# Kernel optimization log

Measured on AMD Instinct MI355X. Metric: run time of the kernel, lower is better.

Reference implementation:

```python
import jax, jax.numpy as jnp
import numpy as np

B, N, E = 8, 10000, 160000
F_IN, HID, EMB = 5, 128, 256
A_LAST, S_STEP = 10, 1


def _gcn_layer(x, src, dst, W, b, num_nodes):
    # PyG GCNConv: h = x @ W^T, add self-loops, symmetric norm, scatter-add, + bias
    h = x @ W.T
    loops = jnp.arange(num_nodes, dtype=src.dtype)
    src2 = jnp.concatenate([src, loops])
    dst2 = jnp.concatenate([dst, loops])
    deg = jax.ops.segment_sum(jnp.ones_like(dst2, dtype=h.dtype), dst2, num_segments=num_nodes)
    dinv = jnp.where(deg > 0, jax.lax.rsqrt(deg), 0.0)
    norm = dinv[src2] * dinv[dst2]                     # [E+N]
    msgs = h[src2] * norm[:, None]                     # gather + scale
    out = jax.ops.segment_sum(msgs, dst2, num_segments=num_nodes)
    return out + b


def setup_inputs() -> dict:
    key = jax.random.key(0)
    ks = jax.random.split(key, 14)
    graph_x = jax.random.normal(ks[0], (B, N, F_IN), dtype=jnp.float32)
    graph_edges = jax.random.randint(ks[1], (B, 2, E), 0, N, dtype=jnp.int64)
    position_seq = jax.random.randint(ks[2], (B,), 0, N, dtype=jnp.int64)
    available_moves = jax.random.randint(ks[3], (B, 4), 0, N, dtype=jnp.int64)
    actions = jax.random.normal(ks[4], (B, A_LAST), dtype=jnp.float32)
    steps = jax.random.normal(ks[5], (B, S_STEP), dtype=jnp.float32)

    def glorot(k, shape):
        fan_in = shape[-1]
        return jax.random.normal(k, shape, dtype=jnp.float32) / jnp.sqrt(jnp.float32(fan_in))

    proj_in = HID * 5 + A_LAST + S_STEP
    params = {
        'W1': glorot(ks[6], (HID, F_IN)), 'b1': jnp.zeros((HID,), jnp.float32),
        'W2': glorot(ks[7], (HID, HID)), 'b2': jnp.zeros((HID,), jnp.float32),
        'Wp1': glorot(ks[8], (EMB, proj_in)), 'bp1': jnp.zeros((EMB,), jnp.float32),
        'Wp2': glorot(ks[9], (EMB, EMB)), 'bp2': jnp.zeros((EMB,), jnp.float32),
    }
    return dict(graph_x=graph_x, graph_edges=graph_edges, position_seq=position_seq,
                available_moves=available_moves, actions=actions, steps=steps, **params)


def reference(graph_x, graph_edges, position_seq, available_moves, actions, steps,
              W1, b1, W2, b2, Wp1, bp1, Wp2, bp2):
    b, n, f = graph_x.shape
    num_nodes = b * n
    x = graph_x.reshape(num_nodes, f)
    addition = (jnp.arange(b, dtype=graph_edges.dtype) * n)
    ei = graph_edges + addition[:, None, None]          # [B,2,E]
    ei = jnp.swapaxes(ei, 0, 1).reshape(2, -1)          # [2, B*E]
    src, dst = ei[0], ei[1]
    position = position_seq + addition
    all_positions = jnp.concatenate(
        [available_moves + addition[:, None], position[:, None]], axis=1)  # [B,5]

    x = jax.nn.relu(_gcn_layer(x, src, dst, W1, b1, num_nodes))
    x = jax.nn.relu(_gcn_layer(x, src, dst, W2, b2, num_nodes))

    current_x = x[all_positions].reshape(b, -1)          # [B, 5*HID]
    current_x = jnp.concatenate([current_x, actions, steps], axis=-1)
    h = jax.nn.relu(current_x @ Wp1.T + bp1)
    return h @ Wp2.T + bp2
```

## Files before the change

kernel.cpp:

```cpp
#include <hip/hip_runtime.h>

#define NB 8
#define NN 10000
#define NE 160000
#define NNODES (NB*NN)
#define NEDGE (NB*NE)
#define FIN 5
#define HID 128
#define EMB 256
#define ALAST 10
#define PROJ_IN (HID*5 + ALAST + 1)
#define NPOS 40
#define E0CAP 256
#define TCAP (NPOS + NPOS*E0CAP)
#define E1C 128
#define NBLK ((NNODES+255)/256)

#define C_NT 0
#define C_E0(t) (8 + (t)*16)

__global__ void k_clear(int* __restrict__ markT, int* __restrict__ degCnt,
                        int* __restrict__ cnts, int* __restrict__ e1cnt) {
    int i = blockIdx.x*256 + threadIdx.x;
    if (i < NNODES) { markT[i] = -1; degCnt[i] = 0; }
    if (i < 1024) cnts[i] = 0;
    for (int j = i; j < TCAP*4; j += NNODES) e1cnt[j] = 0;
}

__global__ void k_mark(const int* __restrict__ avail, const int* __restrict__ pos,
                       int* __restrict__ markT, int* __restrict__ Tnodes,
                       int* __restrict__ cnts,
                       int* __restrict__ pos2t0, int* __restrict__ posNode) {
    int p = threadIdx.x;
    int n = 0;
    if (p < NPOS) {
        int b = p / 5, pi = p - b*5;
        int node = (pi < 4) ? avail[b*4 + pi] : pos[b];
        n = node + b*NN;
    }
    int firstIdx = p;
    for (int q = 0; q < NPOS; ++q) {
        int nq = __shfl(n, q, 64);
        if (p < NPOS && q < p && nq == n && firstIdx == p) firstIdx = q;
    }
    bool isFirst = (p < NPOS) && (firstIdx == p);
    unsigned long long bal = __ballot(isFirst);
    if (p < NPOS) {
        int slot = __popcll(bal & ((1ull << firstIdx) - 1ull));
        if (isFirst) {
            markT[n] = slot; Tnodes[slot] = n;
        }
        pos2t0[p] = slot; posNode[p] = n;
    }
    if (p == 0) cnts[C_NT] = __popcll(bal);
}

__global__ __launch_bounds__(256) void k_pass1(const int* __restrict__ edges,
        const int* __restrict__ markT, int* __restrict__ cnts,
        int* __restrict__ e0) {
    int idx = blockIdx.x*256 + threadIdx.x;
    int g = idx / (NE/4), w4 = idx - g*(NE/4);
    const int* base = edges + (size_t)g*2*NE;
    int4 d4 = ((const int4*)(base + NE))[w4];
    int gofs = g*NN;
    int dd[4] = {d4.x, d4.y, d4.z, d4.w};
    #pragma unroll
    for (int c = 0; c < 4; ++c) {
        int t0 = markT[gofs + dd[c]];
        if (t0 >= 0) {
            int s = base[4*w4 + c] + gofs;
            int k = atomicAdd(&cnts[C_E0(t0)], 1);
            if (k < E0CAP) e0[t0*E0CAP + k] = s;
        }
    }
}

__global__ __launch_bounds__(256) void k_dedup(const int* __restrict__ e0,
                        int* __restrict__ cnts, int* __restrict__ markT,
                        int* __restrict__ Tnodes) {
    __shared__ int lc, base;
    int t0 = blockIdx.x;
    if (threadIdx.x == 0) lc = 0;
    __syncthreads();
    int m = cnts[C_E0(t0)]; if (m > E0CAP) m = E0CAP;
    int s = -1, myIdx = -1;
    if ((int)threadIdx.x < m) {
        s = e0[t0*E0CAP + threadIdx.x];
        if (atomicCAS(&markT[s], -1, -2) == -1)
            myIdx = atomicAdd(&lc, 1);
    }
    __syncthreads();
    if (threadIdx.x == 0 && lc > 0) base = atomicAdd(&cnts[C_NT], lc);
    __syncthreads();
    if (myIdx >= 0) {
        int slot = base + myIdx;
        Tnodes[slot] = s;
        markT[s] = slot;
    }
}

__global__ __launch_bounds__(256) void k_pass2(const int* __restrict__ edges,
        int* __restrict__ markT, int* __restrict__ e1cnt, int* __restrict__ e1,
        int* __restrict__ degCnt) {
    int idx = blockIdx.x*256 + threadIdx.x;
    int g = idx / (NE/4), w4 = idx - g*(NE/4);
    const int* base = edges + (size_t)g*2*NE;
    int4 d4 = ((const int4*)(base + NE))[w4];
    int gofs = g*NN;
    int dd[4] = {d4.x, d4.y, d4.z, d4.w};
    #pragma unroll
    for (int c = 0; c < 4; ++c) {
        int d = gofs + dd[c];
        int ts = markT[d];
        if (ts >= 0) {
            int s = base[4*w4 + c] + gofs;
            int k = atomicAdd(&e1cnt[ts*4], 1);
            if (k < E1C) e1[(size_t)ts*E1C + k] = s;
            atomicAdd(&degCnt[d], 1);
            if (markT[s] == -1) markT[s] = -3;
        }
    }
}

__global__ __launch_bounds__(256) void k_pass3(const int* __restrict__ edges,
        const int* __restrict__ markT, int* __restrict__ degCnt) {
    int idx = blockIdx.x*256 + threadIdx.x;
    int g = idx / (NE/4), w4 = idx - g*(NE/4);
    int4 d4 = ((const int4*)(edges + (size_t)g*2*NE + NE))[w4];
    int gofs = g*NN;
    int dd[4] = {d4.x, d4.y, d4.z, d4.w};
    #pragma unroll
    for (int c = 0; c < 4; ++c) {
        int n = gofs + dd[c];
        if (markT[n] == -3) atomicAdd(&degCnt[n], 1);
    }
}

__global__ __launch_bounds__(256) void k_aggT(
        const int* __restrict__ e1cnt, const int* __restrict__ e1,
        const int* __restrict__ degCnt, const int* __restrict__ cnts,
        const float* __restrict__ xg, float* __restrict__ axT) {
    int slot = blockIdx.x*4 + (threadIdx.x >> 6);
    int lane = threadIdx.x & 63;
    int ntv = cnts[C_NT]; if (ntv > TCAP) ntv = TCAP;
    if (slot >= ntv) return;
    int m = e1cnt[slot*4]; if (m > E1C) m = E1C;
    float acc[FIN] = {0.f, 0.f, 0.f, 0.f, 0.f};
    for (int j = lane; j < m; j += 64) {
        int s = e1[(size_t)slot*E1C + j];
        float dv = rsqrtf(1.0f + (float)degCnt[s]);
        const float* xr = xg + (size_t)s*FIN;
        #pragma unroll
        for (int f = 0; f < FIN; ++f) acc[f] += xr[f]*dv;
    }
    #pragma unroll
    for (int f = 0; f < FIN; ++f) {
        #pragma unroll
        for (int d = 32; d; d >>= 1) acc[f] += __shfl_down(acc[f], d, 64);
    }
    if (lane == 0) {
        #pragma unroll
        for (int f = 0; f < FIN; ++f) axT[(size_t)slot*FIN + f] = acc[f];
    }
}

#define KC 32
__global__ __launch_bounds__(256) void k_h12T(
        const float* __restrict__ axT, const int* __restrict__ Tnodes,
        const int* __restrict__ degCnt, const int* __restrict__ cnts,
        const float* __restrict__ xg,
        const float* __restrict__ W1, const float* __restrict__ b1,
        const float* __restrict__ W2, float* __restrict__ hsT) {
    __shared__ float axs[FIN][128];
    __shared__ float w1s[FIN][128];
    __shared__ float b1s[128];
    __shared__ float dvs[128];
    __shared__ float xs[KC*128];
    __shared__ float wt[KC*64];
    int ntv = cnts[C_NT]; if (ntv > TCAP) ntv = TCAP;
    int jb  = blockIdx.x & 1;
    int m0g = (blockIdx.x >> 1) * 128;
    if (m0g >= ntv) return;
    int tid = threadIdx.x;
    if (tid < 128) {
        b1s[tid] = b1[tid];
        #pragma unroll
        for (int f = 0; f < FIN; ++f) w1s[f][tid] = W1[tid*FIN + f];
    } else {
        int r2 = tid - 128;
        int row = m0g + r2;
        int ok = row < ntv;
        int node = ok ? Tnodes[row] : 0;
        float dvv = ok ? rsqrtf(1.0f + (float)degCnt[node]) : 0.0f;
        dvs[r2] = dvv;
        #pragma unroll
        for (int f = 0; f < FIN; ++f)
            axs[f][r2] = ok ? (axT[(size_t)row*FIN + f]
                               + xg[(size_t)node*FIN + f]*dvv) : 0.0f;
    }
    int tx = tid & 15, ty = tid >> 4;
    int m0 = ty*8;
    int j0 = tx*4;
    int r  = tid >> 1;
    int kq = (tid & 1) * 16;
    int rw  = tid >> 2;
    int kqw = (tid & 3) * 8;
    float a[8][4];
    #pragma unroll
    for (int i = 0; i < 8; ++i)
        #pragma unroll
        for (int j = 0; j < 4; ++j) a[i][j] = 0.f;
    __syncthreads();
    float axr[FIN];
    float dvr = dvs[r];
    #pragma unroll
    for (int f = 0; f < FIN; ++f) axr[f] = axs[f][r] * dvr;

    for (int kh = 0; kh < 128; kh += KC) {
        float4 wv0 = *(const float4*)&W2[(size_t)(jb*64 + rw)*128 + kh + kqw];
        float4 wv1 = *(const float4*)&W2[(size_t)(jb*64 + rw)*128 + kh + kqw + 4];
        float hv[16];
        #pragma unroll
        for (int kk = 0; kk < 16; ++kk) {
            int k1 = kh + kq + kk;
            float sv = b1s[k1];
            #pragma unroll
            for (int f = 0; f < FIN; ++f) sv += axr[f]*w1s[f][k1];
            hv[kk] = fmaxf(sv, 0.0f);
        }
        __syncthreads();
        #pragma unroll
        for (int kk = 0; kk < 16; ++kk) xs[(kq+kk)*128 + r] = hv[kk];
        wt[(kqw+0)*64 + rw] = wv0.x;
        wt[(kqw+1)*64 + rw] = wv0.y;
        wt[(kqw+2)*64 + rw] = wv0.z;
        wt[(kqw+3)*64 + rw] = wv0.w;
        wt[(kqw+4)*64 + rw] = wv1.x;
        wt[(kqw+5)*64 + rw] = wv1.y;
        wt[(kqw+6)*64 + rw] = wv1.z;
        wt[(kqw+7)*64 + rw] = wv1.w;
        __syncthreads();
        for (int k = 0; k < KC; ++k) {
            float4 xa = *(const float4*)&xs[k*128 + m0];
            float4 xb = *(const float4*)&xs[k*128 + m0 + 4];
            float4 wa = *(const float4*)&wt[k*64 + j0];
            float xr[8] = {xa.x,xa.y,xa.z,xa.w,xb.x,xb.y,xb.z,xb.w};
            #pragma unroll
            for (int i = 0; i < 8; ++i) {
                a[i][0] += xr[i]*wa.x;
                a[i][1] += xr[i]*wa.y;
                a[i][2] += xr[i]*wa.z;
                a[i][3] += xr[i]*wa.w;
            }
        }
    }
    #pragma unroll
    for (int i = 0; i < 8; ++i) {
        int row = m0g + m0 + i;
        if (row < ntv) {
            float dv = dvs[m0 + i];
            float4 v0 = make_float4(a[i][0]*dv, a[i][1]*dv, a[i][2]*dv, a[i][3]*dv);
            *(float4*)&hsT[(size_t)row*HID + jb*64 + j0] = v0;
        }
    }
}

__global__ __launch_bounds__(256) void k_mlp1(
        const int* __restrict__ pos2t0, const int* __restrict__ posNode,
        const int* __restrict__ e1cnt, const int* __restrict__ e1,
        const int* __restrict__ markT, const float* __restrict__ hsT,
        const int* __restrict__ degCnt, const float* __restrict__ b2,
        const float* __restrict__ actions, const float* __restrict__ steps,
        const float* __restrict__ Wp1, const float* __restrict__ bp1,
        float* __restrict__ hm) {
    int b  = blockIdx.x >> 4;
    int jg = blockIdx.x & 15;
    int t  = threadIdx.x;
    __shared__ float c[PROJ_IN];
    __shared__ int slots[5*E1C];
    __shared__ int cm[5], t0s[5];
    __shared__ float dvP[5];
    if (t < 5) {
        int t0 = pos2t0[b*5 + t];
        t0s[t] = t0;
        int m = e1cnt[t0*4]; if (m > E1C) m = E1C;
        cm[t] = m;
        dvP[t] = rsqrtf(1.0f + (float)degCnt[posNode[b*5 + t]]);
    }
    __syncthreads();
    for (int i = t; i < 5*E1C; i += 256) {
        int p5 = i >> 7, j = i & (E1C-1);
        if (j < cm[p5]) slots[i] = markT[e1[(size_t)t0s[p5]*E1C + j]];
    }
    __syncthreads();
    for (int i = t; i < 5*HID; i += 256) {
        int p5 = i >> 7, f = i & 127;
        float acc = hsT[(size_t)t0s[p5]*HID + f];
        int m = cm[p5];
        const int* sp = &slots[p5*E1C];
        for (int j = 0; j < m; ++j) {
            int ts = sp[j];
            if (ts >= 0) acc += hsT[(size_t)ts*HID + f];
        }
        c[i] = fmaxf(acc*dvP[p5] + b2[f], 0.0f);
    }
    if (t < ALAST) c[5*HID + t] = actions[b*ALAST + t];
    if (t == ALAST) c[5*HID + ALAST] = steps[b];
    __syncthreads();
    int o = t >> 4, sub = t & 15;
    int j = jg*16 + o;
    const float* wr = Wp1 + (size_t)j*PROJ_IN;
    float s = 0.f;
    for (int k = sub; k < PROJ_IN; k += 16) s += c[k]*wr[k];
    #pragma unroll
    for (int d = 8; d; d >>= 1) s += __shfl_down(s, d, 16);
    if (sub == 0) hm[b*EMB + j] = fmaxf(s + bp1[j], 0.f);
}

__global__ __launch_bounds__(256) void k_mlp2(
        const float* __restrict__ hm, const float* __restrict__ Wp2,
        const float* __restrict__ bp2, float* __restrict__ out) {
    int b  = blockIdx.x >> 4;
    int jg = blockIdx.x & 15;
    int t  = threadIdx.x;
    __shared__ float c[EMB];
    if (t < EMB) c[t] = hm[b*EMB + t];
    __syncthreads();
    int o = t >> 4, sub = t & 15;
    int j = jg*16 + o;
    const float* wr = Wp2 + (size_t)j*EMB;
    float s = 0.f;
    for (int k = sub; k < EMB; k += 16) s += c[k]*wr[k];
    #pragma unroll
    for (int d = 8; d; d >>= 1) s += __shfl_down(s, d, 16);
    if (sub == 0) out[b*EMB + j] = s + bp2[j];
}

extern "C" void kernel_launch(void* const* d_in, const int* in_sizes, int n_in,
                              void* d_out, int out_size, void* d_ws, size_t ws_size,
                              hipStream_t stream) {
    const float* graph_x = (const float*)d_in[0];
    const int*   edges   = (const int*)d_in[1];
    const int*   pos     = (const int*)d_in[2];
    const int*   avail   = (const int*)d_in[3];
    const float* actions = (const float*)d_in[4];
    const float* steps   = (const float*)d_in[5];
    const float* W1  = (const float*)d_in[6];
    const float* b1  = (const float*)d_in[7];
    const float* W2  = (const float*)d_in[8];
    const float* b2  = (const float*)d_in[9];
    const float* Wp1 = (const float*)d_in[10];
    const float* bp1 = (const float*)d_in[11];
    const float* Wp2 = (const float*)d_in[12];
    const float* bp2 = (const float*)d_in[13];
    float* out = (float*)d_out;

    char* ws = (char*)d_ws;
    size_t off = 0;
    #define ALLOC(ptrname, type, nelem) \
        type* ptrname = (type*)(ws + off); off = (off + (size_t)(nelem)*sizeof(type) + 255) & ~(size_t)255;
    ALLOC(markT,   int,   NNODES)
    ALLOC(degCnt,  int,   NNODES)
    ALLOC(cnts,    int,   1024)
    ALLOC(e1cnt,   int,   TCAP*4)
    ALLOC(Tnodes,  int,   TCAP)
    ALLOC(pos2t0,  int,   NPOS)
    ALLOC(posNode, int,   NPOS)
    ALLOC(e0,      int,   NPOS*E0CAP)
    ALLOC(e1,      int,   (size_t)TCAP*E1C)
    ALLOC(axT,     float, (size_t)(TCAP+128)*FIN)
    ALLOC(hsT,     float, (size_t)TCAP*HID)
    ALLOC(hm,      float, (size_t)NB*EMB)
    #undef ALLOC

    k_clear<<<NBLK, 256, 0, stream>>>(markT, degCnt, cnts, e1cnt);
    k_mark<<<1, 64, 0, stream>>>(avail, pos, markT, Tnodes, cnts, pos2t0, posNode);
    k_pass1<<<NEDGE/4/256, 256, 0, stream>>>(edges, markT, cnts, e0);
    k_dedup<<<NPOS, 256, 0, stream>>>(e0, cnts, markT, Tnodes);
    k_pass2<<<NEDGE/4/256, 256, 0, stream>>>(edges, markT, e1cnt, e1, degCnt);
    k_pass3<<<NEDGE/4/256, 256, 0, stream>>>(edges, markT, degCnt);
    k_aggT<<<(TCAP+3)/4, 256, 0, stream>>>(e1cnt, e1, degCnt, cnts, graph_x, axT);
    k_h12T<<<2*((TCAP+127)/128), 256, 0, stream>>>(axT, Tnodes, degCnt, cnts,
                                                   graph_x, W1, b1, W2, hsT);
    k_mlp1<<<NB*16, 256, 0, stream>>>(pos2t0, posNode, e1cnt, e1, markT, hsT,
                                      degCnt, b2, actions, steps, Wp1, bp1, hm);
    k_mlp2<<<NB*16, 256, 0, stream>>>(hm, Wp2, bp2, out);
}
```

Before: 166.5 us.

## Fuse init with mark and compute full in-degree in pass1, dropping pass3

Merges the clear and mark kernels into one init kernel where each block redundantly computes the 40 position slots and writes markT directly. Degree counting moves into pass1 as an unconditional atomicAdd per edge over all nodes, which removes pass3 and the -3 marking in pass2. This cuts two launches and one full scan of the edge list. In exchange pass1 now issues 1.28M global atomics instead of only the conditional ones.

```diff
diff --git a/kernel.cpp b/kernel.cpp
--- a/kernel.cpp
+++ b/kernel.cpp
@@ -19,45 +19,57 @@
 #define C_NT 0
 #define C_E0(t) (8 + (t)*16)
 
-__global__ void k_clear(int* __restrict__ markT, int* __restrict__ degCnt,
-                        int* __restrict__ cnts, int* __restrict__ e1cnt) {
-    int i = blockIdx.x*256 + threadIdx.x;
-    if (i < NNODES) { markT[i] = -1; degCnt[i] = 0; }
-    if (i < 1024) cnts[i] = 0;
+__global__ __launch_bounds__(256) void k_init(
+        const int* __restrict__ avail, const int* __restrict__ pos,
+        int* __restrict__ markT, int* __restrict__ degCnt,
+        int* __restrict__ cnts, int* __restrict__ e1cnt,
+        int* __restrict__ Tnodes, int* __restrict__ pos2t0,
+        int* __restrict__ posNode) {
+    __shared__ int pnode[NPOS];
+    __shared__ int pslot[NPOS];
+    int t = threadIdx.x;
+    if (t < 64) {
+        int p = t, n = -1;
+        if (p < NPOS) {
+            int b = p / 5, pi = p - b*5;
+            int node = (pi < 4) ? avail[b*4 + pi] : pos[b];
+            n = node + b*NN;
+        }
+        int firstIdx = p;
+        for (int q = 0; q < NPOS; ++q) {
+            int nq = __shfl(n, q, 64);
+            if (p < NPOS && q < p && nq == n && firstIdx == p) firstIdx = q;
+        }
+        bool isFirst = (p < NPOS) && (firstIdx == p);
+        unsigned long long bal = __ballot(isFirst);
+        if (p < NPOS) {
+            int slot = __popcll(bal & ((1ull << firstIdx) - 1ull));
+            pnode[p] = n;
+            pslot[p] = slot;
+            if (blockIdx.x == 0) {
+                pos2t0[p] = slot; posNode[p] = n;
+                if (isFirst) Tnodes[slot] = n;
+            }
+        }
+        if (p == 0 && blockIdx.x == 0) cnts[C_NT] = __popcll(bal);
+    }
+    __syncthreads();
+    int i = blockIdx.x*256 + t;
+    if (i < NNODES) {
+        int mk = -1;
+        #pragma unroll
+        for (int p = 0; p < NPOS; ++p)
+            if (i == pnode[p]) mk = pslot[p];
+        markT[i] = mk;
+        degCnt[i] = 0;
+    }
+    if (i >= 1 && i < 1024) cnts[i] = 0;
     for (int j = i; j < TCAP*4; j += NNODES) e1cnt[j] = 0;
-}
-
-__global__ void k_mark(const int* __restrict__ avail, const int* __restrict__ pos,
-                       int* __restrict__ markT, int* __restrict__ Tnodes,
-                       int* __restrict__ cnts,
-                       int* __restrict__ pos2t0, int* __restrict__ posNode) {
-    int p = threadIdx.x;
-    int n = 0;
-    if (p < NPOS) {
-        int b = p / 5, pi = p - b*5;
-        int node = (pi < 4) ? avail[b*4 + pi] : pos[b];
-        n = node + b*NN;
-    }
-    int firstIdx = p;
-    for (int q = 0; q < NPOS; ++q) {
-        int nq = __shfl(n, q, 64);
-        if (p < NPOS && q < p && nq == n && firstIdx == p) firstIdx = q;
-    }
-    bool isFirst = (p < NPOS) && (firstIdx == p);
-    unsigned long long bal = __ballot(isFirst);
-    if (p < NPOS) {
-        int slot = __popcll(bal & ((1ull << firstIdx) - 1ull));
-        if (isFirst) {
-            markT[n] = slot; Tnodes[slot] = n;
-        }
-        pos2t0[p] = slot; posNode[p] = n;
-    }
-    if (p == 0) cnts[C_NT] = __popcll(bal);
 }
 
 __global__ __launch_bounds__(256) void k_pass1(const int* __restrict__ edges,
         const int* __restrict__ markT, int* __restrict__ cnts,
-        int* __restrict__ e0) {
+        int* __restrict__ e0, int* __restrict__ degCnt) {
     int idx = blockIdx.x*256 + threadIdx.x;
     int g = idx / (NE/4), w4 = idx - g*(NE/4);
     const int* base = edges + (size_t)g*2*NE;
@@ -66,7 +78,9 @@
     int dd[4] = {d4.x, d4.y, d4.z, d4.w};
     #pragma unroll
     for (int c = 0; c < 4; ++c) {
-        int t0 = markT[gofs + dd[c]];
+        int d = gofs + dd[c];
+        atomicAdd(&degCnt[d], 1);
+        int t0 = markT[d];
         if (t0 >= 0) {
             int s = base[4*w4 + c] + gofs;
             int k = atomicAdd(&cnts[C_E0(t0)], 1);
@@ -100,8 +114,8 @@
 }
 
 __global__ __launch_bounds__(256) void k_pass2(const int* __restrict__ edges,
-        int* __restrict__ markT, int* __restrict__ e1cnt, int* __restrict__ e1,
-        int* __restrict__ degCnt) {
+        const int* __restrict__ markT, int* __restrict__ e1cnt,
+        int* __restrict__ e1) {
     int idx = blockIdx.x*256 + threadIdx.x;
     int g = idx / (NE/4), w4 = idx - g*(NE/4);
     const int* base = edges + (size_t)g*2*NE;
@@ -110,29 +124,12 @@
     int dd[4] = {d4.x, d4.y, d4.z, d4.w};
     #pragma unroll
     for (int c = 0; c < 4; ++c) {
-        int d = gofs + dd[c];
-        int ts = markT[d];
+        int ts = markT[gofs + dd[c]];
         if (ts >= 0) {
             int s = base[4*w4 + c] + gofs;
             int k = atomicAdd(&e1cnt[ts*4], 1);
             if (k < E1C) e1[(size_t)ts*E1C + k] = s;
-            atomicAdd(&degCnt[d], 1);
-            if (markT[s] == -1) markT[s] = -3;
-        }
-    }
-}
-
-__global__ __launch_bounds__(256) void k_pass3(const int* __restrict__ edges,
-        const int* __restrict__ markT, int* __restrict__ degCnt) {
-    int idx = blockIdx.x*256 + threadIdx.x;
-    int g = idx / (NE/4), w4 = idx - g*(NE/4);
-    int4 d4 = ((const int4*)(edges + (size_t)g*2*NE + NE))[w4];
-    int gofs = g*NN;
-    int dd[4] = {d4.x, d4.y, d4.z, d4.w};
-    #pragma unroll
-    for (int c = 0; c < 4; ++c) {
-        int n = gofs + dd[c];
-        if (markT[n] == -3) atomicAdd(&degCnt[n], 1);
+        }
     }
 }
 
@@ -373,12 +370,11 @@
     ALLOC(hm,      float, (size_t)NB*EMB)
     #undef ALLOC
 
-    k_clear<<<NBLK, 256, 0, stream>>>(markT, degCnt, cnts, e1cnt);
-    k_mark<<<1, 64, 0, stream>>>(avail, pos, markT, Tnodes, cnts, pos2t0, posNode);
-    k_pass1<<<NEDGE/4/256, 256, 0, stream>>>(edges, markT, cnts, e0);
+    k_init<<<NBLK, 256, 0, stream>>>(avail, pos, markT, degCnt, cnts, e1cnt,
+                                     Tnodes, pos2t0, posNode);
+    k_pass1<<<NEDGE/4/256, 256, 0, stream>>>(edges, markT, cnts, e0, degCnt);
     k_dedup<<<NPOS, 256, 0, stream>>>(e0, cnts, markT, Tnodes);
-    k_pass2<<<NEDGE/4/256, 256, 0, stream>>>(edges, markT, e1cnt, e1, degCnt);
-    k_pass3<<<NEDGE/4/256, 256, 0, stream>>>(edges, markT, degCnt);
+    k_pass2<<<NEDGE/4/256, 256, 0, stream>>>(edges, markT, e1cnt, e1);
     k_aggT<<<(TCAP+3)/4, 256, 0, stream>>>(e1cnt, e1, degCnt, cnts, graph_x, axT);
     k_h12T<<<2*((TCAP+127)/128), 256, 0, stream>>>(axT, Tnodes, degCnt, cnts,
                                                    graph_x, W1, b1, W2, hsT);
```

After: 202.4 us. 1.22x slower.
